# Performance work log

Hardware: AMD Instinct MI355X
Metric: run time of the kernel (lower is better)

Reference implementation:

```python
import jax, jax.numpy as jnp
import numpy as np

B, S, D = 4, 2048, 1024

def setup_inputs() -> dict:
    key = jax.random.key(0)
    ks = jax.random.split(key, 10)
    sc = 1.0 / np.sqrt(D)
    return {
        "x": jax.random.normal(ks[0], (B, S, D), dtype=jnp.float32),
        "y": jax.random.normal(ks[1], (B, S, D), dtype=jnp.float32),
        "Wq": jax.random.normal(ks[2], (D, D), dtype=jnp.float32) * sc,
        "bq": jnp.zeros((D,), dtype=jnp.float32),
        "Wk": jax.random.normal(ks[3], (D, D), dtype=jnp.float32) * sc,
        "bk": jnp.zeros((D,), dtype=jnp.float32),
        "Wv": jax.random.normal(ks[4], (D, D), dtype=jnp.float32) * sc,
        "bv": jnp.zeros((D,), dtype=jnp.float32),
        "Wr": jax.random.normal(ks[5], (D, D), dtype=jnp.float32) * sc,
        "br": jnp.zeros((D,), dtype=jnp.float32),
    }

def reference(x, y, Wq, bq, Wk, bk, Wv, bv, Wr, br):
    # Dense projections
    Q = jnp.einsum('bsd,de->bse', x, Wq) + bq
    K = jnp.einsum('bsd,de->bse', y, Wk) + bk
    V = jnp.einsum('bsd,de->bse', y, Wv) + bv
    # learned cosine feature map on keys
    K_hat = jnp.cos(jnp.einsum('bsd,dr->bsr', K, Wr) + br)
    # full softmax attention with feature-mapped keys
    scores = jnp.einsum('bqr,bkr->bqk', Q, K_hat)  # [B, S, S]
    probs = jax.nn.softmax(scores, axis=-1)
    return jnp.einsum('bqk,bkd->bqd', probs, V)
```

## Files before the change

kernel.cpp:

```cpp
#include <hip/hip_runtime.h>
#include <hip/hip_bf16.h>
#include <math.h>

#define B_ 4
#define S_ 2048
#define D_ 1024
#define M_ (B_*S_)
#define MBYTE (1024ull*1024ull)

typedef __attribute__((ext_vector_type(8))) _Float16 f16x8;
typedef __attribute__((ext_vector_type(4))) float f32x4;
typedef __attribute__((ext_vector_type(8))) unsigned short us8;
typedef unsigned short us;

__device__ inline us f2h(float f) {
    union { _Float16 h; us u; } x;
    x.h = (_Float16)f;
    return x.u;
}
__device__ inline float h2f(us u) {
    union { us u; _Float16 h; } x; x.u = u;
    return (float)x.h;
}

__device__ inline void gload16(const us* g, us* l) {
    __builtin_amdgcn_global_load_lds(
        (const __attribute__((address_space(1))) unsigned int*)g,
        (__attribute__((address_space(3))) unsigned int*)l, 16, 0, 0);
}

template<int DO_LO>
__global__ __launch_bounds__(256)
void cast2_k(const float* __restrict__ in, us* __restrict__ hi, us* __restrict__ lo) {
    const size_t i = ((size_t)blockIdx.x * 256 + threadIdx.x) * 4;
    const float4 v = *(const float4*)&in[i];
    ushort4 h;
    h.x = f2h(v.x); h.y = f2h(v.y); h.z = f2h(v.z); h.w = f2h(v.w);
    *(ushort4*)&hi[i] = h;
    if (DO_LO) {
        ushort4 l;
        l.x = f2h(v.x - h2f(h.x)); l.y = f2h(v.y - h2f(h.y));
        l.z = f2h(v.z - h2f(h.z)); l.w = f2h(v.w - h2f(h.w));
        *(ushort4*)&lo[i] = l;
    }
}

template<int DO_LO>
__global__ __launch_bounds__(256)
void wsplit_k(const float* __restrict__ W, us* __restrict__ Wt1, us* __restrict__ Wt2) {
    __shared__ float t[64][65];
    const int tid = threadIdx.x;
    const int k0 = blockIdx.x*64, n0 = blockIdx.y*64;
    #pragma unroll
    for (int i = 0; i < 4; ++i) {
        const int c = i*256 + tid;
        const int row = c >> 4, col = (c & 15) * 4;
        const float4 v = *(const float4*)&W[(size_t)(k0+row)*D_ + n0+col];
        t[row][col]=v.x; t[row][col+1]=v.y; t[row][col+2]=v.z; t[row][col+3]=v.w;
    }
    __syncthreads();
    #pragma unroll
    for (int i = 0; i < 4; ++i) {
        const int c = i*256 + tid;
        const int n = c >> 4, k = (c & 15) * 4;
        float f[4] = { t[k][n], t[k+1][n], t[k+2][n], t[k+3][n] };
        ushort4 h;
        h.x=f2h(f[0]); h.y=f2h(f[1]); h.z=f2h(f[2]); h.w=f2h(f[3]);
        *(ushort4*)&Wt1[(size_t)(n0+n)*D_ + k0+k] = h;
        if (DO_LO) {
            ushort4 l;
            l.x=f2h(f[0]-h2f(h.x)); l.y=f2h(f[1]-h2f(h.y));
            l.z=f2h(f[2]-h2f(h.z)); l.w=f2h(f[3]-h2f(h.w));
            *(ushort4*)&Wt2[(size_t)(n0+n)*D_ + k0+k] = l;
        }
    }
}

__global__ __launch_bounds__(256)
void wreduce_k(const float* __restrict__ Wp, us* __restrict__ W1, us* __restrict__ W2) {
    const size_t i = ((size_t)blockIdx.x * 256 + threadIdx.x) * 4;
    float4 s = *(const float4*)&Wp[i];
    #pragma unroll
    for (int z = 1; z < 8; ++z) {
        const float4 v = *(const float4*)&Wp[(size_t)z*D_*D_ + i];
        s.x += v.x; s.y += v.y; s.z += v.z; s.w += v.w;
    }
    ushort4 h, l;
    h.x=f2h(s.x); h.y=f2h(s.y); h.z=f2h(s.z); h.w=f2h(s.w);
    l.x=f2h(s.x-h2f(h.x)); l.y=f2h(s.y-h2f(h.y));
    l.z=f2h(s.z-h2f(h.z)); l.w=f2h(s.w-h2f(h.w));
    *(ushort4*)&W1[i] = h;
    *(ushort4*)&W2[i] = l;
}

__global__ __launch_bounds__(256)
void bpinit_k(const float* __restrict__ br, float* __restrict__ bp) {
    const int r = blockIdx.x * 256 + threadIdx.x;
    bp[r] = br[r];
}
__global__ __launch_bounds__(256)
void bprime_k(const float* __restrict__ bk, const float* __restrict__ Wr,
              float* __restrict__ bp) {
    const int r = blockIdx.x * 256 + threadIdx.x;
    const int e0 = blockIdx.y * 64;
    float a0 = 0.f, a1 = 0.f, a2 = 0.f, a3 = 0.f;
    for (int e = e0; e < e0 + 64; e += 4) {
        a0 += bk[e+0] * Wr[(size_t)(e+0)*D_ + r];
        a1 += bk[e+1] * Wr[(size_t)(e+1)*D_ + r];
        a2 += bk[e+2] * Wr[(size_t)(e+2)*D_ + r];
        a3 += bk[e+3] * Wr[(size_t)(e+3)*D_ + r];
    }
    atomicAdd(&bp[r], (a0 + a1) + (a2 + a3));
}

template<int Nv, int Kv, int SPLIT, int EPI, int KS>
__global__ __launch_bounds__(256)
void gemm_bt_k(const us* __restrict__ A1, const us* __restrict__ A2,
               const us* __restrict__ B1, const us* __restrict__ B2,
               const float* __restrict__ bias, void* __restrict__ Cv,
               us* __restrict__ C2, long sA, long sB, long sC) {
    __shared__ us smem[(SPLIT?4:2)*128*64];
    us* As  = smem;
    us* As2 = smem + 128*64;
    us* Bs  = smem + (SPLIT?2:1)*128*64;
    us* Bs2 = Bs + 128*64;
    const int tid = threadIdx.x;
    const us* A1b = A1 + (size_t)blockIdx.z * sA;
    const us* A2b = SPLIT ? A2 + (size_t)blockIdx.z * sA : nullptr;
    const us* B1b = B1 + (size_t)blockIdx.z * sB;
    const us* B2b = SPLIT ? B2 + (size_t)blockIdx.z * sB : nullptr;
    const int m0 = blockIdx.x * 128, n0 = blockIdx.y * 128;
    const int lane = tid & 63, w = tid >> 6;
    const int mw = (w >> 1) * 64, nw = (w & 1) * 64;
    const int lr = lane & 15, lq = lane >> 4;

    const int crow = tid >> 3;
    const int ccol = (tid & 7) * 8;

    f32x4 acc[4][4];
    #pragma unroll
    for (int i = 0; i < 4; ++i)
        #pragma unroll
        for (int j = 0; j < 4; ++j)
            acc[i][j] = (f32x4){0.f, 0.f, 0.f, 0.f};

    int kc0 = 0, kc1 = Kv;
    if (KS > 1) {
        const int kchunk = Kv / KS;
        kc0 = blockIdx.z * kchunk;
        kc1 = kc0 + kchunk;
    }
    for (int kc = kc0; kc < kc1; kc += 64) {
        #pragma unroll
        for (int i = 0; i < 4; ++i) {
            const int r = crow + i * 32;
            gload16(&A1b[(size_t)(m0 + r) * Kv + kc + ccol], &As[(size_t)(i*256 + tid) * 8]);
            gload16(&B1b[(size_t)(n0 + r) * Kv + kc + ccol], &Bs[(size_t)(i*256 + tid) * 8]);
            if (SPLIT) {
                gload16(&A2b[(size_t)(m0 + r) * Kv + kc + ccol], &As2[(size_t)(i*256 + tid) * 8]);
                gload16(&B2b[(size_t)(n0 + r) * Kv + kc + ccol], &Bs2[(size_t)(i*256 + tid) * 8]);
            }
        }
        __syncthreads();
        #pragma unroll
        for (int kk = 0; kk < 64; kk += 32) {
            f16x8 a1[4], b1[4];
            #pragma unroll
            for (int i = 0; i < 4; ++i)
                a1[i] = *(const f16x8*)&As[(mw + i*16 + lr) * 64 + kk + lq*8];
            #pragma unroll
            for (int j = 0; j < 4; ++j)
                b1[j] = *(const f16x8*)&Bs[(nw + j*16 + lr) * 64 + kk + lq*8];
            if (SPLIT) {
                f16x8 a2[4], b2[4];
                #pragma unroll
                for (int i = 0; i < 4; ++i)
                    a2[i] = *(const f16x8*)&As2[(mw + i*16 + lr) * 64 + kk + lq*8];
                #pragma unroll
                for (int j = 0; j < 4; ++j)
                    b2[j] = *(const f16x8*)&Bs2[(nw + j*16 + lr) * 64 + kk + lq*8];
                #pragma unroll
                for (int i = 0; i < 4; ++i)
                    #pragma unroll
                    for (int j = 0; j < 4; ++j) {
                        acc[i][j] = __builtin_amdgcn_mfma_f32_16x16x32_f16(a2[i], b1[j], acc[i][j], 0, 0, 0);
                        acc[i][j] = __builtin_amdgcn_mfma_f32_16x16x32_f16(a1[i], b2[j], acc[i][j], 0, 0, 0);
                        acc[i][j] = __builtin_amdgcn_mfma_f32_16x16x32_f16(a1[i], b1[j], acc[i][j], 0, 0, 0);
                    }
            } else {
                #pragma unroll
                for (int i = 0; i < 4; ++i)
                    #pragma unroll
                    for (int j = 0; j < 4; ++j)
                        acc[i][j] = __builtin_amdgcn_mfma_f32_16x16x32_f16(a1[i], b1[j], acc[i][j], 0, 0, 0);
            }
        }
        __syncthreads();
    }

    float* slab = (float*)smem + (size_t)w * 2048;
    const int lrow0 = lane >> 3, cb = (lane & 7) * 8;
    #pragma unroll
    for (int p = 0; p < 2; ++p) {
        #pragma unroll
        for (int ii = 0; ii < 2; ++ii) {
            const int i = p*2 + ii;
            #pragma unroll
            for (int j = 0; j < 4; ++j)
                #pragma unroll
                for (int r = 0; r < 4; ++r)
                    slab[(ii*16 + lq*4 + r)*64 + j*16 + lr] = acc[i][j][r];
        }
        __syncthreads();
        #pragma unroll
        for (int t = 0; t < 4; ++t) {
            const int lrow = t*8 + lrow0;
            const int grow = m0 + mw + p*32 + lrow;
            const int gcol = n0 + nw + cb;
            const size_t idx = (size_t)grow * Nv + gcol;
            float v[8];
            #pragma unroll
            for (int u = 0; u < 8; ++u) v[u] = slab[lrow*64 + cb + u];
            if (EPI == 0) {
                float* Cf = (float*)Cv + (size_t)blockIdx.z * sC;
                float4 o0 = {v[0],v[1],v[2],v[3]}, o1 = {v[4],v[5],v[6],v[7]};
                *(float4*)&Cf[idx] = o0;
                *(float4*)&Cf[idx+4] = o1;
            } else if (EPI == 1 || EPI == 2) {
                us* Ch = (us*)Cv + (size_t)blockIdx.z * sC;
                us8 o;
                #pragma unroll
                for (int u = 0; u < 8; ++u) {
                    const float tv = v[u] + (bias ? bias[gcol + u] : 0.f);
                    o[u] = f2h(EPI == 2 ? cosf(tv) : tv);
                }
                *(us8*)&Ch[idx] = o;
            } else if (EPI == 4) {
                us* Ch = (us*)Cv + (size_t)blockIdx.z * sC;
                const float rb = bias ? bias[grow] : 0.f;
                us8 o;
                #pragma unroll
                for (int u = 0; u < 8; ++u) o[u] = f2h(v[u] + rb);
                *(us8*)&Ch[idx] = o;
            } else {
                us* Ch  = (us*)Cv + (size_t)blockIdx.z * sC;
                us* C2h = C2 + (size_t)blockIdx.z * sC;
                us8 oh, ol;
                #pragma unroll
                for (int u = 0; u < 8; ++u) {
                    const float tv = v[u] + (bias ? bias[gcol + u] : 0.f);
                    const us hh = f2h(tv);
                    oh[u] = hh;
                    ol[u] = f2h(tv - h2f(hh));
                }
                *(us8*)&Ch[idx] = oh;
                *(us8*)&C2h[idx] = ol;
            }
        }
        __syncthreads();
    }
}

__global__ __launch_bounds__(256)
void softmax_k(const float* __restrict__ S, us* __restrict__ P) {
    __shared__ float red[8];
    const int tid = threadIdx.x;
    const int lane = tid & 63, w = tid >> 6;
    const float* row = S + (size_t)blockIdx.x * S_;

    const float4 v0 = *(const float4*)&row[tid*8];
    const float4 v1 = *(const float4*)&row[tid*8 + 4];
    float e[8] = {v0.x, v0.y, v0.z, v0.w, v1.x, v1.y, v1.z, v1.w};

    float mx = e[0];
    #pragma unroll
    for (int j = 1; j < 8; ++j) mx = fmaxf(mx, e[j]);
    #pragma unroll
    for (int off = 1; off < 64; off <<= 1) mx = fmaxf(mx, __shfl_xor(mx, off));
    if (lane == 0) red[w] = mx;
    __syncthreads();
    mx = fmaxf(fmaxf(red[0], red[1]), fmaxf(red[2], red[3]));

    float sum = 0.f;
    #pragma unroll
    for (int j = 0; j < 8; ++j) { e[j] = __expf(e[j] - mx); sum += e[j]; }
    #pragma unroll
    for (int off = 1; off < 64; off <<= 1) sum += __shfl_xor(sum, off);
    if (lane == 0) red[4 + w] = sum;
    __syncthreads();
    const float inv = 1.0f / (red[4] + red[5] + red[6] + red[7]);

    us8 o;
    #pragma unroll
    for (int j = 0; j < 8; ++j) o[j] = f2h(e[j] * inv);
    *(us8*)&P[(size_t)blockIdx.x * S_ + tid*8] = o;
}

extern "C" void kernel_launch(void* const* d_in, const int* in_sizes, int n_in,
                              void* d_out, int out_size, void* d_ws, size_t ws_size,
                              hipStream_t stream) {
    const float* x  = (const float*)d_in[0];
    const float* y  = (const float*)d_in[1];
    const float* Wq = (const float*)d_in[2];
    const float* bq = (const float*)d_in[3];
    const float* Wk = (const float*)d_in[4];
    const float* bk = (const float*)d_in[5];
    const float* Wv = (const float*)d_in[6];
    const float* bv = (const float*)d_in[7];
    const float* Wr = (const float*)d_in[8];
    const float* br = (const float*)d_in[9];
    float* out = (float*)d_out;

    char* wsb = (char*)d_ws;
    us*    y1   = (us*)(wsb +  0*MBYTE);
    us*    y2   = (us*)(wsb + 16*MBYTE);
    us*    xh   = (us*)(wsb + 16*MBYTE);
    us*    Pb   = (us*)(wsb + 16*MBYTE);
    float* Wp   = (float*)(wsb + 32*MBYTE);
    us*    Qb   = (us*)(wsb + 32*MBYTE);
    us*    P23  = (us*)(wsb + 32*MBYTE);
    us*    Kh   = (us*)(wsb + 48*MBYTE);
    us*    Wkf1 = (us*)(wsb + 64*MBYTE);
    us*    Wkf2 = (us*)(wsb + 66*MBYTE);
    us*    Wr1  = (us*)(wsb + 68*MBYTE);
    us*    Wr2  = (us*)(wsb + 70*MBYTE);
    us*    WT1  = (us*)(wsb + 72*MBYTE);
    us*    WT2  = (us*)(wsb + 74*MBYTE);
    float* bp   = (float*)(wsb + 76*MBYTE);
    us*    Wq1  = (us*)(wsb + 64*MBYTE);
    float* S2   = (float*)(wsb + 64*MBYTE);
    us*    Vt   = (us*)(wsb + 64*MBYTE);
    us*    Wv1  = (us*)(wsb + 80*MBYTE);

    const dim3 bb(256);
    const dim3 gcast(M_*D_/1024), gcastW(D_*D_/1024), gw(16,16);
    const dim3 gproj(M_/128, D_/128);

    cast2_k<1><<<gcast, bb, 0, stream>>>(y, y1, y2);
    cast2_k<1><<<gcastW, bb, 0, stream>>>(Wk, Wkf1, Wkf2);
    wsplit_k<1><<<gw, bb, 0, stream>>>(Wr, Wr1, Wr2);
    bpinit_k<<<dim3(D_/256), bb, 0, stream>>>(br, bp);
    bprime_k<<<dim3(D_/256, 16), bb, 0, stream>>>(bk, Wr, bp);
    gemm_bt_k<D_, D_, 1, 0, 8><<<dim3(D_/128, D_/128, 8), bb, 0, stream>>>(
        Wr1, Wr2, Wkf1, Wkf2, nullptr, (void*)Wp, nullptr,
        0, 0, (long)D_*D_);
    wreduce_k<<<dim3(D_*D_/1024), bb, 0, stream>>>(Wp, WT1, WT2);
    gemm_bt_k<D_, D_, 1, 2, 1><<<gproj, bb, 0, stream>>>(
        y1, y2, WT1, WT2, bp, (void*)Kh, nullptr, 0, 0, 0);

    cast2_k<0><<<gcast, bb, 0, stream>>>(x, xh, nullptr);
    wsplit_k<0><<<gw, bb, 0, stream>>>(Wq, Wq1, nullptr);
    gemm_bt_k<D_, D_, 0, 1, 1><<<gproj, bb, 0, stream>>>(
        xh, nullptr, Wq1, nullptr, bq, (void*)Qb, nullptr, 0, 0, 0);

    gemm_bt_k<S_, D_, 0, 0, 1><<<dim3(S_/128, S_/128, 2), bb, 0, stream>>>(
        Qb, nullptr, Kh, nullptr,
        nullptr, (void*)S2, nullptr, (long)S_*D_, (long)S_*D_, (long)S_*S_);
    softmax_k<<<dim3(2*S_), bb, 0, stream>>>(S2, Pb);
    gemm_bt_k<S_, D_, 0, 0, 1><<<dim3(S_/128, S_/128, 2), bb, 0, stream>>>(
        Qb + 2*(size_t)S_*D_, nullptr, Kh + 2*(size_t)S_*D_, nullptr,
        nullptr, (void*)S2, nullptr, (long)S_*D_, (long)S_*D_, (long)S_*S_);
    softmax_k<<<dim3(2*S_), bb, 0, stream>>>(S2, P23);

    wsplit_k<0><<<gw, bb, 0, stream>>>(Wv, Wv1, nullptr);
    gemm_bt_k<S_, D_, 0, 4, 1><<<dim3(D_/128, S_/128, B_), bb, 0, stream>>>(
        Wv1, nullptr, y1, nullptr, bv, (void*)Vt, nullptr,
        0, (long)S_*D_, (long)D_*S_);

    gemm_bt_k<D_, S_, 0, 0, 1><<<dim3(S_/128, D_/128, B_), bb, 0, stream>>>(
        Pb, nullptr, Vt, nullptr, nullptr, (void*)out, nullptr,
        (long)S_*S_, (long)D_*S_, (long)S_*D_);
}
```

Measured before the change: 489.4 us.

## Split K-feature projection into correction GEMM plus main GEMM with cosine epilogue

The split-precision K-hat projection, which carried both hi and lo operands through one SPLIT GEMM, is replaced by two GEMMs. The first computes only the cross terms (y1·WT2 + y2·WT1) by concatenating them along K and writes fp32 to a scratch buffer. The second does the main y1·WT1 product and adds the scratch, the bias and the cosine in a new epilogue. This shrinks per-block shared memory for the projection, which may raise occupancy, at the cost of an extra launch and an fp32 intermediate written and read. The workspace layout is reshuffled to fit the new buffer.

```diff
diff --git a/kernel.cpp b/kernel.cpp
--- a/kernel.cpp
+++ b/kernel.cpp
@@ -113,12 +113,13 @@
     atomicAdd(&bp[r], (a0 + a1) + (a2 + a3));
 }
 
-template<int Nv, int Kv, int SPLIT, int EPI, int KS>
+template<int Nv, int Kv, int SPLIT, int EPI, int KS, int XK>
 __global__ __launch_bounds__(256)
 void gemm_bt_k(const us* __restrict__ A1, const us* __restrict__ A2,
                const us* __restrict__ B1, const us* __restrict__ B2,
-               const float* __restrict__ bias, void* __restrict__ Cv,
-               us* __restrict__ C2, long sA, long sB, long sC) {
+               const float* __restrict__ bias, const float* __restrict__ Cin,
+               void* __restrict__ Cv, us* __restrict__ C2,
+               long sA, long sB, long sC) {
     __shared__ us smem[(SPLIT?4:2)*128*64];
     us* As  = smem;
     us* As2 = smem + 128*64;
@@ -126,9 +127,9 @@
     us* Bs2 = Bs + 128*64;
     const int tid = threadIdx.x;
     const us* A1b = A1 + (size_t)blockIdx.z * sA;
-    const us* A2b = SPLIT ? A2 + (size_t)blockIdx.z * sA : nullptr;
+    const us* A2b = (SPLIT||XK) ? A2 + (size_t)blockIdx.z * sA : nullptr;
     const us* B1b = B1 + (size_t)blockIdx.z * sB;
-    const us* B2b = SPLIT ? B2 + (size_t)blockIdx.z * sB : nullptr;
+    const us* B2b = (SPLIT||XK) ? B2 + (size_t)blockIdx.z * sB : nullptr;
     const int m0 = blockIdx.x * 128, n0 = blockIdx.y * 128;
     const int lane = tid & 63, w = tid >> 6;
     const int mw = (w >> 1) * 64, nw = (w & 1) * 64;
@@ -144,21 +145,28 @@
         for (int j = 0; j < 4; ++j)
             acc[i][j] = (f32x4){0.f, 0.f, 0.f, 0.f};
 
-    int kc0 = 0, kc1 = Kv;
+    int kc0 = 0, kc1 = XK ? 2*Kv : Kv;
     if (KS > 1) {
         const int kchunk = Kv / KS;
         kc0 = blockIdx.z * kchunk;
         kc1 = kc0 + kchunk;
     }
     for (int kc = kc0; kc < kc1; kc += 64) {
+        const us* Ab = A1b; const us* Bb = B1b; int ko = kc;
+        if (XK) {
+            const bool s1 = kc >= Kv;
+            Ab = s1 ? A2b : A1b;
+            Bb = s1 ? B1b : B2b;
+            ko = s1 ? kc - Kv : kc;
+        }
         #pragma unroll
         for (int i = 0; i < 4; ++i) {
             const int r = crow + i * 32;
-            gload16(&A1b[(size_t)(m0 + r) * Kv + kc + ccol], &As[(size_t)(i*256 + tid) * 8]);
-            gload16(&B1b[(size_t)(n0 + r) * Kv + kc + ccol], &Bs[(size_t)(i*256 + tid) * 8]);
+            gload16(&Ab[(size_t)(m0 + r) * Kv + ko + ccol], &As[(size_t)(i*256 + tid) * 8]);
+            gload16(&Bb[(size_t)(n0 + r) * Kv + ko + ccol], &Bs[(size_t)(i*256 + tid) * 8]);
             if (SPLIT) {
-                gload16(&A2b[(size_t)(m0 + r) * Kv + kc + ccol], &As2[(size_t)(i*256 + tid) * 8]);
-                gload16(&B2b[(size_t)(n0 + r) * Kv + kc + ccol], &Bs2[(size_t)(i*256 + tid) * 8]);
+                gload16(&A2b[(size_t)(m0 + r) * Kv + ko + ccol], &As2[(size_t)(i*256 + tid) * 8]);
+                gload16(&B2b[(size_t)(n0 + r) * Kv + ko + ccol], &Bs2[(size_t)(i*256 + tid) * 8]);
             }
         }
         __syncthreads();
@@ -242,6 +250,18 @@
                 #pragma unroll
                 for (int u = 0; u < 8; ++u) o[u] = f2h(v[u] + rb);
                 *(us8*)&Ch[idx] = o;
+            } else if (EPI == 6) {
+                us* Ch = (us*)Cv + (size_t)blockIdx.z * sC;
+                const float4 c0 = *(const float4*)&Cin[idx];
+                const float4 c1 = *(const float4*)&Cin[idx + 4];
+                const float ca[8] = {c0.x,c0.y,c0.z,c0.w,c1.x,c1.y,c1.z,c1.w};
+                us8 o;
+                #pragma unroll
+                for (int u = 0; u < 8; ++u) {
+                    const float tv = v[u] + ca[u] + (bias ? bias[gcol + u] : 0.f);
+                    o[u] = f2h(cosf(tv));
+                }
+                *(us8*)&Ch[idx] = o;
             } else {
                 us* Ch  = (us*)Cv + (size_t)blockIdx.z * sC;
                 us* C2h = C2 + (size_t)blockIdx.z * sC;
@@ -316,21 +336,22 @@
     us*    y2   = (us*)(wsb + 16*MBYTE);
     us*    xh   = (us*)(wsb + 16*MBYTE);
     us*    Pb   = (us*)(wsb + 16*MBYTE);
-    float* Wp   = (float*)(wsb + 32*MBYTE);
-    us*    Qb   = (us*)(wsb + 32*MBYTE);
+    us*    Kh   = (us*)(wsb + 32*MBYTE);
     us*    P23  = (us*)(wsb + 32*MBYTE);
-    us*    Kh   = (us*)(wsb + 48*MBYTE);
-    us*    Wkf1 = (us*)(wsb + 64*MBYTE);
-    us*    Wkf2 = (us*)(wsb + 66*MBYTE);
-    us*    Wr1  = (us*)(wsb + 68*MBYTE);
-    us*    Wr2  = (us*)(wsb + 70*MBYTE);
-    us*    WT1  = (us*)(wsb + 72*MBYTE);
-    us*    WT2  = (us*)(wsb + 74*MBYTE);
-    float* bp   = (float*)(wsb + 76*MBYTE);
-    us*    Wq1  = (us*)(wsb + 64*MBYTE);
+    float* Wp   = (float*)(wsb + 48*MBYTE);
+    float* X32  = (float*)(wsb + 48*MBYTE);
+    us*    Qb   = (us*)(wsb + 48*MBYTE);
+    us*    Vt   = (us*)(wsb + 48*MBYTE);
     float* S2   = (float*)(wsb + 64*MBYTE);
-    us*    Vt   = (us*)(wsb + 64*MBYTE);
+    us*    Wq1  = (us*)(wsb + 80*MBYTE);
     us*    Wv1  = (us*)(wsb + 80*MBYTE);
+    float* bp   = (float*)(wsb + 82*MBYTE);
+    us*    WT1  = (us*)(wsb + 84*MBYTE);
+    us*    WT2  = (us*)(wsb + 86*MBYTE);
+    us*    Wkf1 = (us*)(wsb + 88*MBYTE);
+    us*    Wkf2 = (us*)(wsb + 90*MBYTE);
+    us*    Wr1  = (us*)(wsb + 92*MBYTE);
+    us*    Wr2  = (us*)(wsb + 94*MBYTE);
 
     const dim3 bb(256);
     const dim3 gcast(M_*D_/1024), gcastW(D_*D_/1024), gw(16,16);
@@ -341,33 +362,37 @@
     wsplit_k<1><<<gw, bb, 0, stream>>>(Wr, Wr1, Wr2);
     bpinit_k<<<dim3(D_/256), bb, 0, stream>>>(br, bp);
     bprime_k<<<dim3(D_/256, 16), bb, 0, stream>>>(bk, Wr, bp);
-    gemm_bt_k<D_, D_, 1, 0, 8><<<dim3(D_/128, D_/128, 8), bb, 0, stream>>>(
-        Wr1, Wr2, Wkf1, Wkf2, nullptr, (void*)Wp, nullptr,
+    gemm_bt_k<D_, D_, 1, 0, 8, 0><<<dim3(D_/128, D_/128, 8), bb, 0, stream>>>(
+        Wr1, Wr2, Wkf1, Wkf2, nullptr, nullptr, (void*)Wp, nullptr,
         0, 0, (long)D_*D_);
     wreduce_k<<<dim3(D_*D_/1024), bb, 0, stream>>>(Wp, WT1, WT2);
-    gemm_bt_k<D_, D_, 1, 2, 1><<<gproj, bb, 0, stream>>>(
-        y1, y2, WT1, WT2, bp, (void*)Kh, nullptr, 0, 0, 0);
+
+    gemm_bt_k<D_, D_, 0, 0, 1, 1><<<gproj, bb, 0, stream>>>(
+        y1, y2, WT1, WT2, nullptr, nullptr, (void*)X32, nullptr, 0, 0, 0);
+    gemm_bt_k<D_, D_, 0, 6, 1, 0><<<gproj, bb, 0, stream>>>(
+        y1, nullptr, WT1, nullptr, bp, X32, (void*)Kh, nullptr, 0, 0, 0);
 
     cast2_k<0><<<gcast, bb, 0, stream>>>(x, xh, nullptr);
     wsplit_k<0><<<gw, bb, 0, stream>>>(Wq, Wq1, nullptr);
-    gemm_bt_k<D_, D_, 0, 1, 1><<<gproj, bb, 0, stream>>>(
-        xh, nullptr, Wq1, nullptr, bq, (void*)Qb, nullptr, 0, 0, 0);
-
-    gemm_bt_k<S_, D_, 0, 0, 1><<<dim3(S_/128, S_/128, 2), bb, 0, stream>>>(
-        Qb, nullptr, Kh, nullptr,
-        nullptr, (void*)S2, nullptr, (long)S_*D_, (long)S_*D_, (long)S_*S_);
+    gemm_bt_k<D_, D_, 0, 1, 1, 0><<<gproj, bb, 0, stream>>>(
+        xh, nullptr, Wq1, nullptr, bq, nullptr, (void*)Qb, nullptr, 0, 0, 0);
+
+    gemm_bt_k<S_, D_, 0, 0, 1, 0><<<dim3(S_/128, S_/128, 2), bb, 0, stream>>>(
+        Qb, nullptr, Kh, nullptr, nullptr, nullptr,
+        (void*)S2, nullptr, (long)S_*D_, (long)S_*D_, (long)S_*S_);
     softmax_k<<<dim3(2*S_), bb, 0, stream>>>(S2, Pb);
-    gemm_bt_k<S_, D_, 0, 0, 1><<<dim3(S_/128, S_/128, 2), bb, 0, stream>>>(
+    gemm_bt_k<S_, D_, 0, 0, 1, 0><<<dim3(S_/128, S_/128, 2), bb, 0, stream>>>(
         Qb + 2*(size_t)S_*D_, nullptr, Kh + 2*(size_t)S_*D_, nullptr,
-        nullptr, (void*)S2, nullptr, (long)S_*D_, (long)S_*D_, (long)S_*S_);
+        nullptr, nullptr,
+        (void*)S2, nullptr, (long)S_*D_, (long)S_*D_, (long)S_*S_);
     softmax_k<<<dim3(2*S_), bb, 0, stream>>>(S2, P23);
 
     wsplit_k<0><<<gw, bb, 0, stream>>>(Wv, Wv1, nullptr);
-    gemm_bt_k<S_, D_, 0, 4, 1><<<dim3(D_/128, S_/128, B_), bb, 0, stream>>>(
-        Wv1, nullptr, y1, nullptr, bv, (void*)Vt, nullptr,
+    gemm_bt_k<S_, D_, 0, 4, 1, 0><<<dim3(D_/128, S_/128, B_), bb, 0, stream>>>(
+        Wv1, nullptr, y1, nullptr, bv, nullptr, (void*)Vt, nullptr,
         0, (long)S_*D_, (long)D_*S_);
 
-    gemm_bt_k<D_, S_, 0, 0, 1><<<dim3(S_/128, D_/128, B_), bb, 0, stream>>>(
-        Pb, nullptr, Vt, nullptr, nullptr, (void*)out, nullptr,
+    gemm_bt_k<D_, S_, 0, 0, 1, 0><<<dim3(S_/128, D_/128, B_), bb, 0, stream>>>(
+        Pb, nullptr, Vt, nullptr, nullptr, nullptr, (void*)out, nullptr,
         (long)S_*S_, (long)D_*S_, (long)S_*D_);
 }
```

Measured after the change: 527.1 us. 1.08x slower.

## Double-buffer shared-memory tiles in the GEMM main loop

Applied to the files above, without the earlier changes.

The GEMM kernel gets two shared-memory buffers. The next K-slice is staged while the current one is computed, with one barrier per iteration instead of two. For the split (hi/lo) variant the K-step drops from 64 to 32 to fit in shared memory. The unused hi/lo-split epilogue and its C2 argument are removed. This trades higher LDS use, which may reduce occupancy, for overlap of global loads with MFMA work.

```diff
diff --git a/kernel.cpp b/kernel.cpp
--- a/kernel.cpp
+++ b/kernel.cpp
@@ -118,12 +118,11 @@
 void gemm_bt_k(const us* __restrict__ A1, const us* __restrict__ A2,
                const us* __restrict__ B1, const us* __restrict__ B2,
                const float* __restrict__ bias, void* __restrict__ Cv,
-               us* __restrict__ C2, long sA, long sB, long sC) {
-    __shared__ us smem[(SPLIT?4:2)*128*64];
-    us* As  = smem;
-    us* As2 = smem + 128*64;
-    us* Bs  = smem + (SPLIT?2:1)*128*64;
-    us* Bs2 = Bs + 128*64;
+               long sA, long sB, long sC) {
+    constexpr int BK   = SPLIT ? 32 : 64;
+    constexpr int NMAT = SPLIT ? 4 : 2;
+    constexpr int BUFE = NMAT * 128 * BK;
+    __shared__ us smem[2 * BUFE];
     const int tid = threadIdx.x;
     const us* A1b = A1 + (size_t)blockIdx.z * sA;
     const us* A2b = SPLIT ? A2 + (size_t)blockIdx.z * sA : nullptr;
@@ -134,8 +133,9 @@
     const int mw = (w >> 1) * 64, nw = (w & 1) * 64;
     const int lr = lane & 15, lq = lane >> 4;
 
-    const int crow = tid >> 3;
-    const int ccol = (tid & 7) * 8;
+    constexpr int SI = BK / 16;
+    const int srow = tid / (BK/8);
+    const int scol = (tid % (BK/8)) * 8;
 
     f32x4 acc[4][4];
     #pragma unroll
@@ -150,35 +150,44 @@
         kc0 = blockIdx.z * kchunk;
         kc1 = kc0 + kchunk;
     }
-    for (int kc = kc0; kc < kc1; kc += 64) {
-        #pragma unroll
-        for (int i = 0; i < 4; ++i) {
-            const int r = crow + i * 32;
-            gload16(&A1b[(size_t)(m0 + r) * Kv + kc + ccol], &As[(size_t)(i*256 + tid) * 8]);
-            gload16(&B1b[(size_t)(n0 + r) * Kv + kc + ccol], &Bs[(size_t)(i*256 + tid) * 8]);
+
+    auto STAGE = [&](int b, int kc) {
+        us* dst = smem + b * BUFE;
+        #pragma unroll
+        for (int i = 0; i < SI; ++i) {
+            const int r = srow + i * (128 / SI);
+            const size_t off = (size_t)(i*256 + tid) * 8;
+            gload16(&A1b[(size_t)(m0 + r) * Kv + kc + scol], &dst[off]);
+            gload16(&B1b[(size_t)(n0 + r) * Kv + kc + scol], &dst[128*BK + off]);
             if (SPLIT) {
-                gload16(&A2b[(size_t)(m0 + r) * Kv + kc + ccol], &As2[(size_t)(i*256 + tid) * 8]);
-                gload16(&B2b[(size_t)(n0 + r) * Kv + kc + ccol], &Bs2[(size_t)(i*256 + tid) * 8]);
+                gload16(&A2b[(size_t)(m0 + r) * Kv + kc + scol], &dst[2*128*BK + off]);
+                gload16(&B2b[(size_t)(n0 + r) * Kv + kc + scol], &dst[3*128*BK + off]);
             }
         }
-        __syncthreads();
-        #pragma unroll
-        for (int kk = 0; kk < 64; kk += 32) {
+    };
+
+    auto COMPUTE = [&](int b) {
+        const us* As_  = smem + b * BUFE;
+        const us* Bs_  = As_ + 128*BK;
+        const us* As2_ = As_ + 2*128*BK;
+        const us* Bs2_ = As_ + 3*128*BK;
+        #pragma unroll
+        for (int kk = 0; kk < BK; kk += 32) {
             f16x8 a1[4], b1[4];
             #pragma unroll
             for (int i = 0; i < 4; ++i)
-                a1[i] = *(const f16x8*)&As[(mw + i*16 + lr) * 64 + kk + lq*8];
+                a1[i] = *(const f16x8*)&As_[(mw + i*16 + lr) * BK + kk + lq*8];
             #pragma unroll
             for (int j = 0; j < 4; ++j)
-                b1[j] = *(const f16x8*)&Bs[(nw + j*16 + lr) * 64 + kk + lq*8];
+                b1[j] = *(const f16x8*)&Bs_[(nw + j*16 + lr) * BK + kk + lq*8];
             if (SPLIT) {
                 f16x8 a2[4], b2[4];
                 #pragma unroll
                 for (int i = 0; i < 4; ++i)
-                    a2[i] = *(const f16x8*)&As2[(mw + i*16 + lr) * 64 + kk + lq*8];
+                    a2[i] = *(const f16x8*)&As2_[(mw + i*16 + lr) * BK + kk + lq*8];
                 #pragma unroll
                 for (int j = 0; j < 4; ++j)
-                    b2[j] = *(const f16x8*)&Bs2[(nw + j*16 + lr) * 64 + kk + lq*8];
+                    b2[j] = *(const f16x8*)&Bs2_[(nw + j*16 + lr) * BK + kk + lq*8];
                 #pragma unroll
                 for (int i = 0; i < 4; ++i)
                     #pragma unroll
@@ -195,7 +204,16 @@
                         acc[i][j] = __builtin_amdgcn_mfma_f32_16x16x32_f16(a1[i], b1[j], acc[i][j], 0, 0, 0);
             }
         }
+    };
+
+    STAGE(0, kc0);
+    __syncthreads();
+    int cur = 0;
+    for (int kc = kc0; kc < kc1; kc += BK) {
+        if (kc + BK < kc1) STAGE(cur ^ 1, kc + BK);
+        COMPUTE(cur);
         __syncthreads();
+        cur ^= 1;
     }
 
     float* slab = (float*)smem + (size_t)w * 2048;
@@ -235,26 +253,13 @@
                     o[u] = f2h(EPI == 2 ? cosf(tv) : tv);
                 }
                 *(us8*)&Ch[idx] = o;
-            } else if (EPI == 4) {
+            } else {
                 us* Ch = (us*)Cv + (size_t)blockIdx.z * sC;
                 const float rb = bias ? bias[grow] : 0.f;
                 us8 o;
                 #pragma unroll
                 for (int u = 0; u < 8; ++u) o[u] = f2h(v[u] + rb);
                 *(us8*)&Ch[idx] = o;
-            } else {
-                us* Ch  = (us*)Cv + (size_t)blockIdx.z * sC;
-                us* C2h = C2 + (size_t)blockIdx.z * sC;
-                us8 oh, ol;
-                #pragma unroll
-                for (int u = 0; u < 8; ++u) {
-                    const float tv = v[u] + (bias ? bias[gcol + u] : 0.f);
-                    const us hh = f2h(tv);
-                    oh[u] = hh;
-                    ol[u] = f2h(tv - h2f(hh));
-                }
-                *(us8*)&Ch[idx] = oh;
-                *(us8*)&C2h[idx] = ol;
             }
         }
         __syncthreads();
@@ -342,32 +347,32 @@
     bpinit_k<<<dim3(D_/256), bb, 0, stream>>>(br, bp);
     bprime_k<<<dim3(D_/256, 16), bb, 0, stream>>>(bk, Wr, bp);
     gemm_bt_k<D_, D_, 1, 0, 8><<<dim3(D_/128, D_/128, 8), bb, 0, stream>>>(
-        Wr1, Wr2, Wkf1, Wkf2, nullptr, (void*)Wp, nullptr,
-        0, 0, (long)D_*D_);
+        Wr1, Wr2, Wkf1, Wkf2, nullptr, (void*)Wp, 0, 0, (long)D_*D_);
     wreduce_k<<<dim3(D_*D_/1024), bb, 0, stream>>>(Wp, WT1, WT2);
+
     gemm_bt_k<D_, D_, 1, 2, 1><<<gproj, bb, 0, stream>>>(
-        y1, y2, WT1, WT2, bp, (void*)Kh, nullptr, 0, 0, 0);
+        y1, y2, WT1, WT2, bp, (void*)Kh, 0, 0, 0);
 
     cast2_k<0><<<gcast, bb, 0, stream>>>(x, xh, nullptr);
     wsplit_k<0><<<gw, bb, 0, stream>>>(Wq, Wq1, nullptr);
     gemm_bt_k<D_, D_, 0, 1, 1><<<gproj, bb, 0, stream>>>(
-        xh, nullptr, Wq1, nullptr, bq, (void*)Qb, nullptr, 0, 0, 0);
+        xh, nullptr, Wq1, nullptr, bq, (void*)Qb, 0, 0, 0);
 
     gemm_bt_k<S_, D_, 0, 0, 1><<<dim3(S_/128, S_/128, 2), bb, 0, stream>>>(
-        Qb, nullptr, Kh, nullptr,
-        nullptr, (void*)S2, nullptr, (long)S_*D_, (long)S_*D_, (long)S_*S_);
+        Qb, nullptr, Kh, nullptr, nullptr,
+        (void*)S2, (long)S_*D_, (long)S_*D_, (long)S_*S_);
     softmax_k<<<dim3(2*S_), bb, 0, stream>>>(S2, Pb);
     gemm_bt_k<S_, D_, 0, 0, 1><<<dim3(S_/128, S_/128, 2), bb, 0, stream>>>(
-        Qb + 2*(size_t)S_*D_, nullptr, Kh + 2*(size_t)S_*D_, nullptr,
-        nullptr, (void*)S2, nullptr, (long)S_*D_, (long)S_*D_, (long)S_*S_);
+        Qb + 2*(size_t)S_*D_, nullptr, Kh + 2*(size_t)S_*D_, nullptr, nullptr,
+        (void*)S2, (long)S_*D_, (long)S_*D_, (long)S_*S_);
     softmax_k<<<dim3(2*S_), bb, 0, stream>>>(S2, P23);
 
     wsplit_k<0><<<gw, bb, 0, stream>>>(Wv, Wv1, nullptr);
     gemm_bt_k<S_, D_, 0, 4, 1><<<dim3(D_/128, S_/128, B_), bb, 0, stream>>>(
-        Wv1, nullptr, y1, nullptr, bv, (void*)Vt, nullptr,
+        Wv1, nullptr, y1, nullptr, bv, (void*)Vt,
         0, (long)S_*D_, (long)D_*S_);
 
     gemm_bt_k<D_, S_, 0, 0, 1><<<dim3(S_/128, D_/128, B_), bb, 0, stream>>>(
-        Pb, nullptr, Vt, nullptr, nullptr, (void*)out, nullptr,
+        Pb, nullptr, Vt, nullptr, nullptr, (void*)out,
         (long)S_*S_, (long)D_*S_, (long)S_*D_);
 }
```

Measured after the change: 530.2 us. 8.3% more time.
